# Kernel tuning notes

Measured on AMD Instinct MI355X. Metric: run time of the kernel, lower is better.

## Reference

```python
import jax, jax.numpy as jnp
import numpy as np

B, S, D = 2, 2048, 1024
H = 16
DH = D // H  # 64

def setup_inputs() -> dict:
    key = jax.random.key(0)
    k1, k2, k3, k4 = jax.random.split(key, 4)
    scale = 0.02
    x = jax.random.normal(k1, (B, S, D), dtype=jnp.float32)
    W_query = jax.random.normal(k2, (D, D), dtype=jnp.float32) * scale
    W_key = jax.random.normal(k3, (D, D), dtype=jnp.float32) * scale
    W_value = jax.random.normal(k4, (D, D), dtype=jnp.float32) * scale
    return {"x": x, "W_query": W_query, "W_key": W_key, "W_value": W_value}

def reference(x, W_query, W_key, W_value):
    b, n, d_in = x.shape
    # project and split heads: [b, h, n, dh]
    q = (x @ W_query).reshape(b, n, H, DH).transpose(0, 2, 1, 3)
    k = (x @ W_key).reshape(b, n, H, DH).transpose(0, 2, 1, 3)
    v = (x @ W_value).reshape(b, n, H, DH).transpose(0, 2, 1, 3)
    # raw scores, then causal mask (strict upper triangle -> -inf)
    scores = jnp.einsum('bhqd,bhkd->bhqk', q, k)
    causal = jnp.tril(jnp.ones((n, n), dtype=bool))  # True = keep
    scores = jnp.where(causal, scores, -jnp.inf)
    weights = jax.nn.softmax(scores / jnp.sqrt(jnp.float32(DH)), axis=-1)
    ctx = jnp.einsum('bhqk,bhkd->bhqd', weights, v)
    return ctx.transpose(0, 2, 1, 3).reshape(b, n, H * DH)
```

## Files before the change

kernel.cpp:

```cpp
#include <hip/hip_runtime.h>
#include <hip/hip_bf16.h>

#define S_LEN   2048
#define D_MODEL 1024
#define N_HEADS 16
#define D_HEAD  64
#define HEAD_ELEMS (2048ull * 64ull)
#define MAT_ELEMS  (4096ull * 1024ull)
#define W_ELEMS    (1024ull * 1024ull)

typedef __attribute__((ext_vector_type(8))) short short8_t;
typedef __attribute__((ext_vector_type(4))) short short4_t;
typedef __attribute__((ext_vector_type(4))) float f32x4;

__device__ __forceinline__ short f2bf(float f) {
    __hip_bfloat16 h = __float2bfloat16(f);
    union { __hip_bfloat16 h; short s; } cv;
    cv.h = h;
    return cv.s;
}

#define GLD_LDS16(gptr, lptr) \
    __builtin_amdgcn_global_load_lds( \
        (const __attribute__((address_space(1))) unsigned int*)(gptr), \
        (__attribute__((address_space(3))) unsigned int*)(lptr), 16, 0, 0)

__global__ __launch_bounds__(256) void convert_x_kernel(
    const float* __restrict__ x, short* __restrict__ xb)
{
    const int i = (blockIdx.x * 256 + threadIdx.x) * 8;
    const float4 v0 = *(const float4*)(x + i);
    const float4 v1 = *(const float4*)(x + i + 4);
    short8_t u;
    u[0] = f2bf(v0.x); u[1] = f2bf(v0.y); u[2] = f2bf(v0.z); u[3] = f2bf(v0.w);
    u[4] = f2bf(v1.x); u[5] = f2bf(v1.y); u[6] = f2bf(v1.z); u[7] = f2bf(v1.w);
    *(short8_t*)(xb + i) = u;
}

__global__ __launch_bounds__(256) void transpose_w_kernel(
    const float* __restrict__ Wq, const float* __restrict__ Wk,
    const float* __restrict__ Wv, short* __restrict__ wt)
{
    const int k0 = blockIdx.x * 64;
    const int n0 = blockIdx.y * 64;
    const int which = blockIdx.z;
    const float* W = (which == 0) ? Wq : (which == 1) ? Wk : Wv;
    short* out = wt + (size_t)which * W_ELEMS;

    __shared__ float Ts[64][68];
    const int t = threadIdx.x;
    {
        const int c4 = (t & 15) * 4;
#pragma unroll
        for (int i = 0; i < 4; ++i) {
            const int r = (t >> 4) + i * 16;
            const float4 v = *(const float4*)(W + (size_t)(k0 + r) * D_MODEL + n0 + c4);
            Ts[c4 + 0][r] = v.x; Ts[c4 + 1][r] = v.y;
            Ts[c4 + 2][r] = v.z; Ts[c4 + 3][r] = v.w;
        }
    }
    __syncthreads();
    const int nl = t >> 2;
#pragma unroll
    for (int s = 0; s < 2; ++s) {
        const int koff = (t & 3) * 8 + s * 32;
        short8_t u;
#pragma unroll
        for (int j = 0; j < 8; ++j) u[j] = f2bf(Ts[nl][koff + j]);
        *(short8_t*)(out + (size_t)(n0 + nl) * D_MODEL + k0 + koff) = u;
    }
}

__global__ __launch_bounds__(256, 3) void qkv_mfma_gemm_kernel(
    const short* __restrict__ xb,
    const short* __restrict__ wt,
    short* __restrict__ qkv)
{
    const int mBlock = blockIdx.x * 128;
    const int nBlock = blockIdx.y * 128;
    const int which  = blockIdx.z;
    const short* Bt = wt + (size_t)which * W_ELEMS;
    short* outBase  = qkv + (size_t)which * MAT_ELEMS;

    __shared__ short As[128 * 32];
    __shared__ short Bs[128 * 32];

    const int t    = threadIdx.x;
    const int w    = t >> 6;
    const int lane = t & 63;
    const int n16  = lane & 15;
    const int quad = lane >> 4;
    const int mq   = (w & 1) * 64;
    const int nq   = (w >> 1) * 64;

    f32x4 acc[4][4];
#pragma unroll
    for (int i = 0; i < 4; ++i)
#pragma unroll
        for (int j = 0; j < 4; ++j) acc[i][j] = (f32x4){0.f, 0.f, 0.f, 0.f};

    const int off0 = w * 2048 + lane * 16;
    const int off1 = off0 + 1024;
    const int r0s = off0 >> 6, k0s = (off0 & 63) >> 1;
    const int r1s = off1 >> 6, k1s = (off1 & 63) >> 1;
    const short* gA0 = xb + (size_t)(mBlock + r0s) * D_MODEL + k0s;
    const short* gA1 = xb + (size_t)(mBlock + r1s) * D_MODEL + k1s;
    const short* gB0 = Bt + (size_t)(nBlock + r0s) * D_MODEL + k0s;
    const short* gB1 = Bt + (size_t)(nBlock + r1s) * D_MODEL + k1s;
    short* lA0 = As + w * 1024;
    short* lA1 = As + w * 1024 + 512;
    short* lB0 = Bs + w * 1024;
    short* lB1 = Bs + w * 1024 + 512;

    for (int k0 = 0; k0 < D_MODEL; k0 += 32) {
        __syncthreads();
        GLD_LDS16(gA0 + k0, lA0);
        GLD_LDS16(gA1 + k0, lA1);
        GLD_LDS16(gB0 + k0, lB0);
        GLD_LDS16(gB1 + k0, lB1);
        __syncthreads();

        short8_t af[4], bf[4];
#pragma unroll
        for (int mt = 0; mt < 4; ++mt)
            af[mt] = *(const short8_t*)&As[(mq + mt * 16 + n16) * 32 + quad * 8];
#pragma unroll
        for (int nt = 0; nt < 4; ++nt)
            bf[nt] = *(const short8_t*)&Bs[(nq + nt * 16 + n16) * 32 + quad * 8];
#pragma unroll
        for (int mt = 0; mt < 4; ++mt)
#pragma unroll
            for (int nt = 0; nt < 4; ++nt)
                acc[mt][nt] = __builtin_amdgcn_mfma_f32_16x16x32_bf16(
                    af[mt], bf[nt], acc[mt][nt], 0, 0, 0);
    }

    const float oscale = (which == 0) ? 0.125f : 1.0f;
    if (which < 2) {
#pragma unroll
        for (int mt = 0; mt < 4; ++mt) {
#pragma unroll
            for (int nt = 0; nt < 4; ++nt) {
                const int n = nBlock + nq + nt * 16 + n16;
                const int h = n >> 6, dh = n & 63;
#pragma unroll
                for (int reg = 0; reg < 4; ++reg) {
                    const int m = mBlock + mq + mt * 16 + quad * 4 + reg;
                    const int bb = m >> 11, ss = m & 2047;
                    outBase[((size_t)(bb * N_HEADS + h) * S_LEN + ss) * D_HEAD + dh] =
                        f2bf(acc[mt][nt][reg] * oscale);
                }
            }
        }
    } else {
#pragma unroll
        for (int mt = 0; mt < 4; ++mt) {
            const int m0 = mBlock + mq + mt * 16 + quad * 4;
            const int bb = m0 >> 11, ss0 = m0 & 2047;
#pragma unroll
            for (int nt = 0; nt < 4; ++nt) {
                const int n = nBlock + nq + nt * 16 + n16;
                const int h = n >> 6, dh = n & 63;
                short4_t u;
                u[0] = f2bf(acc[mt][nt][0]); u[1] = f2bf(acc[mt][nt][1]);
                u[2] = f2bf(acc[mt][nt][2]); u[3] = f2bf(acc[mt][nt][3]);
                *(short4_t*)(outBase +
                    ((size_t)((bb * N_HEADS + h) * D_HEAD + dh)) * S_LEN + ss0) = u;
            }
        }
    }
}

__global__ __launch_bounds__(256, 2) void attn_mfma_kernel(
    const short* __restrict__ qkv,
    float* __restrict__ out)
{
    const int bh   = blockIdx.x;
    const int pr   = blockIdx.y;
    const int t    = threadIdx.x;
    const int w    = t >> 6;
    const int lane = t & 63;
    const int n    = lane & 15;
    const int quad = lane >> 4;

    const short* Q  = qkv + (size_t)bh * HEAD_ELEMS;
    const short* K  = qkv + MAT_ELEMS + (size_t)bh * HEAD_ELEMS;
    const short* Vt = qkv + 2 * MAT_ELEMS + (size_t)bh * HEAD_ELEMS;

    __shared__ __align__(16) short Ks[64 * 64];
    __shared__ __align__(16) short Vs[64 * 64];
    __shared__ __align__(16) short Ps[4][16][72];

    const int srow0 = w * 16 + (lane >> 3);
    const int srow1 = srow0 + 8;
    const int sd0 = ((lane & 7) ^ (srow0 & 7)) * 8;
    const int sd1 = ((lane & 7) ^ (srow1 & 7)) * 8;
    const short* gK0 = K + srow0 * 64 + sd0;
    const short* gK1 = K + srow1 * 64 + sd1;
    const short* gV0 = Vt + (size_t)srow0 * S_LEN + sd0;
    const short* gV1 = Vt + (size_t)srow1 * S_LEN + sd1;
    short* lK0 = Ks + (w * 16) * 64;
    short* lK1 = Ks + (w * 16 + 8) * 64;
    short* lV0 = Vs + (w * 16) * 64;
    short* lV1 = Vs + (w * 16 + 8) * 64;

    const int pcK = ((quad ^ (n & 7))) * 8;

    const int bb = bh >> 4;
    const int hh = bh & 15;

    for (int pass = 0; pass < 2; ++pass) {
        const int qb = pass ? (31 - pr) : pr;
        const int r0 = qb * 64 + w * 16;
        const int qrow = r0 + n;

        const short8_t bq0 = *(const short8_t*)(Q + (size_t)qrow * D_HEAD + quad * 8);
        const short8_t bq1 = *(const short8_t*)(Q + (size_t)qrow * D_HEAD + quad * 8 + 32);

        float m = -__builtin_inff();
        float l = 0.f;
        f32x4 o[4];
#pragma unroll
        for (int f = 0; f < 4; ++f) o[f] = (f32x4){0.f, 0.f, 0.f, 0.f};

        for (int tile = 0; tile <= qb; ++tile) {
            const int j0 = tile * 64;
            __syncthreads();
            GLD_LDS16(gK0 + j0 * 64, lK0);
            GLD_LDS16(gK1 + j0 * 64, lK1);
            GLD_LDS16(gV0 + j0, lV0);
            GLD_LDS16(gV1 + j0, lV1);
            __syncthreads();

            f32x4 st[4];
#pragma unroll
            for (int kg = 0; kg < 4; ++kg) {
                const int rbase = (kg * 16 + n) * 64;
                const short8_t a0 = *(const short8_t*)&Ks[rbase + pcK];
                const short8_t a1 = *(const short8_t*)&Ks[rbase + (pcK ^ 32)];
                f32x4 acc = (f32x4){0.f, 0.f, 0.f, 0.f};
                acc = __builtin_amdgcn_mfma_f32_16x16x32_bf16(a0, bq0, acc, 0, 0, 0);
                acc = __builtin_amdgcn_mfma_f32_16x16x32_bf16(a1, bq1, acc, 0, 0, 0);
                st[kg] = acc;
            }

            float p[16];
            float mx = -__builtin_inff();
            if (tile == qb) {
#pragma unroll
                for (int kg = 0; kg < 4; ++kg)
#pragma unroll
                    for (int r = 0; r < 4; ++r) {
                        const int key = j0 + kg * 16 + quad * 4 + r;
                        float s = st[kg][r];
                        s = (key <= qrow) ? s : -__builtin_inff();
                        p[kg * 4 + r] = s;
                        mx = fmaxf(mx, s);
                    }
            } else {
#pragma unroll
                for (int i = 0; i < 16; ++i) {
                    const float s = st[i >> 2][i & 3];
                    p[i] = s;
                    mx = fmaxf(mx, s);
                }
            }
            mx = fmaxf(mx, __shfl_xor(mx, 16));
            mx = fmaxf(mx, __shfl_xor(mx, 32));
            const float mnew  = fmaxf(m, mx);
            const float alpha = __expf(m - mnew);
            float ls = 0.f;
#pragma unroll
            for (int i = 0; i < 16; ++i) {
                p[i] = __expf(p[i] - mnew);
                ls += p[i];
            }
            ls += __shfl_xor(ls, 16);
            ls += __shfl_xor(ls, 32);
            l = l * alpha + ls;
            m = mnew;
#pragma unroll
            for (int f = 0; f < 4; ++f) {
                o[f][0] *= alpha; o[f][1] *= alpha; o[f][2] *= alpha; o[f][3] *= alpha;
            }

#pragma unroll
            for (int kg = 0; kg < 4; ++kg) {
                const unsigned int b0 = __builtin_bit_cast(unsigned int, p[kg * 4 + 0]);
                const unsigned int b1 = __builtin_bit_cast(unsigned int, p[kg * 4 + 1]);
                const unsigned int b2 = __builtin_bit_cast(unsigned int, p[kg * 4 + 2]);
                const unsigned int b3 = __builtin_bit_cast(unsigned int, p[kg * 4 + 3]);
                uint2 pk;
                pk.x = (b0 >> 16) | (b1 & 0xffff0000u);
                pk.y = (b2 >> 16) | (b3 & 0xffff0000u);
                *(uint2*)&Ps[w][n][kg * 16 + quad * 4] = pk;
            }
            const short8_t pb0 = *(const short8_t*)&Ps[w][n][quad * 8];
            const short8_t pb1 = *(const short8_t*)&Ps[w][n][quad * 8 + 32];

#pragma unroll
            for (int f = 0; f < 4; ++f) {
                const int rbase = (f * 16 + n) * 64;
                const short8_t va0 = *(const short8_t*)&Vs[rbase + pcK];
                const short8_t va1 = *(const short8_t*)&Vs[rbase + (pcK ^ 32)];
                o[f] = __builtin_amdgcn_mfma_f32_16x16x32_bf16(va0, pb0, o[f], 0, 0, 0);
                o[f] = __builtin_amdgcn_mfma_f32_16x16x32_bf16(va1, pb1, o[f], 0, 0, 0);
            }
        }

        __syncthreads();
        float* Os = (float*)((w < 2) ? Ks : Vs) + (w & 1) * 1024;
        const float inv_l = 1.0f / l;
#pragma unroll
        for (int f = 0; f < 4; ++f) {
            const int c  = f * 4 + quad;
            const int pc = c ^ n;
            f32x4 q4;
            q4[0] = o[f][0] * inv_l; q4[1] = o[f][1] * inv_l;
            q4[2] = o[f][2] * inv_l; q4[3] = o[f][3] * inv_l;
            *(f32x4*)&Os[n * 64 + pc * 4] = q4;
        }
#pragma unroll
        for (int rr = 0; rr < 4; ++rr) {
            const int row = rr * 4 + quad;
            const int pc  = n ^ row;
            const f32x4 val = *(const f32x4*)&Os[row * 64 + pc * 4];
            *(f32x4*)(out + ((size_t)(bb * S_LEN + r0 + row)) * D_MODEL
                          + hh * D_HEAD + n * 4) = val;
        }
    }
}

extern "C" void kernel_launch(void* const* d_in, const int* in_sizes, int n_in,
                              void* d_out, int out_size, void* d_ws, size_t ws_size,
                              hipStream_t stream) {
    const float* x  = (const float*)d_in[0];
    const float* Wq = (const float*)d_in[1];
    const float* Wk = (const float*)d_in[2];
    const float* Wv = (const float*)d_in[3];
    float* out = (float*)d_out;

    short* xb  = (short*)d_ws;
    short* wt  = xb + MAT_ELEMS;
    short* qkv = wt + 3 * W_ELEMS;

    convert_x_kernel<<<dim3(MAT_ELEMS / (256 * 8)), 256, 0, stream>>>(x, xb);
    transpose_w_kernel<<<dim3(16, 16, 3), 256, 0, stream>>>(Wq, Wk, Wv, wt);

    qkv_mfma_gemm_kernel<<<dim3(32, 8, 3), 256, 0, stream>>>(xb, wt, qkv);

    attn_mfma_kernel<<<dim3(2 * N_HEADS, 16), 256, 0, stream>>>(qkv, out);
}
```

Before: 153.7 us.

## Swap MFMA operands for Q/K vectorized stores; one query block per attention CTA

For the Q and K projections, the GEMM swaps the MFMA A/B operands so each lane holds four consecutive head-dim values and can write them as one 8-byte store, replacing four scalar bf16 stores. The attention kernel drops its two-pass pairing of query blocks (pr and 31-pr) and launches one CTA per query block, 32 per head, raising launch_bounds occupancy to 4. This gives more, shorter CTAs and more concurrency, but workloads become unbalanced under the causal mask, so tail effects depend on scheduling.

```diff
diff --git a/kernel.cpp b/kernel.cpp
--- a/kernel.cpp
+++ b/kernel.cpp
@@ -112,6 +112,7 @@
     short* lB0 = Bs + w * 1024;
     short* lB1 = Bs + w * 1024 + 512;
 
+    const bool swapOp = (which < 2);
     for (int k0 = 0; k0 < D_MODEL; k0 += 32) {
         __syncthreads();
         GLD_LDS16(gA0 + k0, lA0);
@@ -127,29 +128,40 @@
 #pragma unroll
         for (int nt = 0; nt < 4; ++nt)
             bf[nt] = *(const short8_t*)&Bs[(nq + nt * 16 + n16) * 32 + quad * 8];
-#pragma unroll
-        for (int mt = 0; mt < 4; ++mt)
-#pragma unroll
-            for (int nt = 0; nt < 4; ++nt)
-                acc[mt][nt] = __builtin_amdgcn_mfma_f32_16x16x32_bf16(
-                    af[mt], bf[nt], acc[mt][nt], 0, 0, 0);
-    }
-
-    const float oscale = (which == 0) ? 0.125f : 1.0f;
+        if (swapOp) {
+#pragma unroll
+            for (int mt = 0; mt < 4; ++mt)
+#pragma unroll
+                for (int nt = 0; nt < 4; ++nt)
+                    acc[mt][nt] = __builtin_amdgcn_mfma_f32_16x16x32_bf16(
+                        bf[nt], af[mt], acc[mt][nt], 0, 0, 0);
+        } else {
+#pragma unroll
+            for (int mt = 0; mt < 4; ++mt)
+#pragma unroll
+                for (int nt = 0; nt < 4; ++nt)
+                    acc[mt][nt] = __builtin_amdgcn_mfma_f32_16x16x32_bf16(
+                        af[mt], bf[nt], acc[mt][nt], 0, 0, 0);
+        }
+    }
+
     if (which < 2) {
-#pragma unroll
-        for (int mt = 0; mt < 4; ++mt) {
-#pragma unroll
-            for (int nt = 0; nt < 4; ++nt) {
-                const int n = nBlock + nq + nt * 16 + n16;
-                const int h = n >> 6, dh = n & 63;
-#pragma unroll
-                for (int reg = 0; reg < 4; ++reg) {
-                    const int m = mBlock + mq + mt * 16 + quad * 4 + reg;
-                    const int bb = m >> 11, ss = m & 2047;
-                    outBase[((size_t)(bb * N_HEADS + h) * S_LEN + ss) * D_HEAD + dh] =
-                        f2bf(acc[mt][nt][reg] * oscale);
-                }
+        const float oscale = (which == 0) ? 0.125f : 1.0f;
+#pragma unroll
+        for (int nt = 0; nt < 4; ++nt) {
+            const int nBase = nBlock + nq + nt * 16 + quad * 4;
+            const int h = nBase >> 6, dh0 = nBase & 63;
+#pragma unroll
+            for (int mt = 0; mt < 4; ++mt) {
+                const int mrow = mBlock + mq + mt * 16 + n16;
+                const int bb = mrow >> 11, ss = mrow & 2047;
+                short4_t u;
+                u[0] = f2bf(acc[mt][nt][0] * oscale);
+                u[1] = f2bf(acc[mt][nt][1] * oscale);
+                u[2] = f2bf(acc[mt][nt][2] * oscale);
+                u[3] = f2bf(acc[mt][nt][3] * oscale);
+                *(short4_t*)(outBase +
+                    ((size_t)(bb * N_HEADS + h) * S_LEN + ss) * D_HEAD + dh0) = u;
             }
         }
     } else {
@@ -171,12 +183,12 @@
     }
 }
 
-__global__ __launch_bounds__(256, 2) void attn_mfma_kernel(
+__global__ __launch_bounds__(256, 4) void attn_mfma_kernel(
     const short* __restrict__ qkv,
     float* __restrict__ out)
 {
     const int bh   = blockIdx.x;
-    const int pr   = blockIdx.y;
+    const int qb   = blockIdx.y;
     const int t    = threadIdx.x;
     const int w    = t >> 6;
     const int lane = t & 63;
@@ -204,130 +216,127 @@
     short* lV0 = Vs + (w * 16) * 64;
     short* lV1 = Vs + (w * 16 + 8) * 64;
 
-    const int pcK = ((quad ^ (n & 7))) * 8;
+    const int pcK = (quad ^ (n & 7)) * 8;
 
     const int bb = bh >> 4;
     const int hh = bh & 15;
 
-    for (int pass = 0; pass < 2; ++pass) {
-        const int qb = pass ? (31 - pr) : pr;
-        const int r0 = qb * 64 + w * 16;
-        const int qrow = r0 + n;
-
-        const short8_t bq0 = *(const short8_t*)(Q + (size_t)qrow * D_HEAD + quad * 8);
-        const short8_t bq1 = *(const short8_t*)(Q + (size_t)qrow * D_HEAD + quad * 8 + 32);
-
-        float m = -__builtin_inff();
-        float l = 0.f;
-        f32x4 o[4];
-#pragma unroll
-        for (int f = 0; f < 4; ++f) o[f] = (f32x4){0.f, 0.f, 0.f, 0.f};
-
-        for (int tile = 0; tile <= qb; ++tile) {
-            const int j0 = tile * 64;
-            __syncthreads();
-            GLD_LDS16(gK0 + j0 * 64, lK0);
-            GLD_LDS16(gK1 + j0 * 64, lK1);
-            GLD_LDS16(gV0 + j0, lV0);
-            GLD_LDS16(gV1 + j0, lV1);
-            __syncthreads();
-
-            f32x4 st[4];
-#pragma unroll
-            for (int kg = 0; kg < 4; ++kg) {
-                const int rbase = (kg * 16 + n) * 64;
-                const short8_t a0 = *(const short8_t*)&Ks[rbase + pcK];
-                const short8_t a1 = *(const short8_t*)&Ks[rbase + (pcK ^ 32)];
-                f32x4 acc = (f32x4){0.f, 0.f, 0.f, 0.f};
-                acc = __builtin_amdgcn_mfma_f32_16x16x32_bf16(a0, bq0, acc, 0, 0, 0);
-                acc = __builtin_amdgcn_mfma_f32_16x16x32_bf16(a1, bq1, acc, 0, 0, 0);
-                st[kg] = acc;
-            }
-
-            float p[16];
-            float mx = -__builtin_inff();
-            if (tile == qb) {
-#pragma unroll
-                for (int kg = 0; kg < 4; ++kg)
-#pragma unroll
-                    for (int r = 0; r < 4; ++r) {
-                        const int key = j0 + kg * 16 + quad * 4 + r;
-                        float s = st[kg][r];
-                        s = (key <= qrow) ? s : -__builtin_inff();
-                        p[kg * 4 + r] = s;
-                        mx = fmaxf(mx, s);
-                    }
-            } else {
-#pragma unroll
-                for (int i = 0; i < 16; ++i) {
-                    const float s = st[i >> 2][i & 3];
-                    p[i] = s;
+    const int r0 = qb * 64 + w * 16;
+    const int qrow = r0 + n;
+
+    const short8_t bq0 = *(const short8_t*)(Q + (size_t)qrow * D_HEAD + quad * 8);
+    const short8_t bq1 = *(const short8_t*)(Q + (size_t)qrow * D_HEAD + quad * 8 + 32);
+
+    float m = -__builtin_inff();
+    float l = 0.f;
+    f32x4 o[4];
+#pragma unroll
+    for (int f = 0; f < 4; ++f) o[f] = (f32x4){0.f, 0.f, 0.f, 0.f};
+
+    for (int tile = 0; tile <= qb; ++tile) {
+        const int j0 = tile * 64;
+        __syncthreads();
+        GLD_LDS16(gK0 + j0 * 64, lK0);
+        GLD_LDS16(gK1 + j0 * 64, lK1);
+        GLD_LDS16(gV0 + j0, lV0);
+        GLD_LDS16(gV1 + j0, lV1);
+        __syncthreads();
+
+        f32x4 st[4];
+#pragma unroll
+        for (int kg = 0; kg < 4; ++kg) {
+            const int rbase = (kg * 16 + n) * 64;
+            const short8_t a0 = *(const short8_t*)&Ks[rbase + pcK];
+            const short8_t a1 = *(const short8_t*)&Ks[rbase + (pcK ^ 32)];
+            f32x4 acc = (f32x4){0.f, 0.f, 0.f, 0.f};
+            acc = __builtin_amdgcn_mfma_f32_16x16x32_bf16(a0, bq0, acc, 0, 0, 0);
+            acc = __builtin_amdgcn_mfma_f32_16x16x32_bf16(a1, bq1, acc, 0, 0, 0);
+            st[kg] = acc;
+        }
+
+        float p[16];
+        float mx = -__builtin_inff();
+        if (tile == qb) {
+#pragma unroll
+            for (int kg = 0; kg < 4; ++kg)
+#pragma unroll
+                for (int r = 0; r < 4; ++r) {
+                    const int key = j0 + kg * 16 + quad * 4 + r;
+                    float s = st[kg][r];
+                    s = (key <= qrow) ? s : -__builtin_inff();
+                    p[kg * 4 + r] = s;
                     mx = fmaxf(mx, s);
                 }
+        } else {
+#pragma unroll
+            for (int i = 0; i < 16; ++i) {
+                const float s = st[i >> 2][i & 3];
+                p[i] = s;
+                mx = fmaxf(mx, s);
             }
-            mx = fmaxf(mx, __shfl_xor(mx, 16));
-            mx = fmaxf(mx, __shfl_xor(mx, 32));
-            const float mnew  = fmaxf(m, mx);
-            const float alpha = __expf(m - mnew);
-            float ls = 0.f;
-#pragma unroll
-            for (int i = 0; i < 16; ++i) {
-                p[i] = __expf(p[i] - mnew);
-                ls += p[i];
-            }
-            ls += __shfl_xor(ls, 16);
-            ls += __shfl_xor(ls, 32);
-            l = l * alpha + ls;
-            m = mnew;
-#pragma unroll
-            for (int f = 0; f < 4; ++f) {
-                o[f][0] *= alpha; o[f][1] *= alpha; o[f][2] *= alpha; o[f][3] *= alpha;
-            }
-
-#pragma unroll
-            for (int kg = 0; kg < 4; ++kg) {
-                const unsigned int b0 = __builtin_bit_cast(unsigned int, p[kg * 4 + 0]);
-                const unsigned int b1 = __builtin_bit_cast(unsigned int, p[kg * 4 + 1]);
-                const unsigned int b2 = __builtin_bit_cast(unsigned int, p[kg * 4 + 2]);
-                const unsigned int b3 = __builtin_bit_cast(unsigned int, p[kg * 4 + 3]);
-                uint2 pk;
-                pk.x = (b0 >> 16) | (b1 & 0xffff0000u);
-                pk.y = (b2 >> 16) | (b3 & 0xffff0000u);
-                *(uint2*)&Ps[w][n][kg * 16 + quad * 4] = pk;
-            }
-            const short8_t pb0 = *(const short8_t*)&Ps[w][n][quad * 8];
-            const short8_t pb1 = *(const short8_t*)&Ps[w][n][quad * 8 + 32];
-
-#pragma unroll
-            for (int f = 0; f < 4; ++f) {
-                const int rbase = (f * 16 + n) * 64;
-                const short8_t va0 = *(const short8_t*)&Vs[rbase + pcK];
-                const short8_t va1 = *(const short8_t*)&Vs[rbase + (pcK ^ 32)];
-                o[f] = __builtin_amdgcn_mfma_f32_16x16x32_bf16(va0, pb0, o[f], 0, 0, 0);
-                o[f] = __builtin_amdgcn_mfma_f32_16x16x32_bf16(va1, pb1, o[f], 0, 0, 0);
-            }
-        }
-
-        __syncthreads();
-        float* Os = (float*)((w < 2) ? Ks : Vs) + (w & 1) * 1024;
-        const float inv_l = 1.0f / l;
+        }
+        mx = fmaxf(mx, __shfl_xor(mx, 16));
+        mx = fmaxf(mx, __shfl_xor(mx, 32));
+        const float mnew  = fmaxf(m, mx);
+        const float alpha = __expf(m - mnew);
+        float ls = 0.f;
+#pragma unroll
+        for (int i = 0; i < 16; ++i) {
+            p[i] = __expf(p[i] - mnew);
+            ls += p[i];
+        }
+        ls += __shfl_xor(ls, 16);
+        ls += __shfl_xor(ls, 32);
+        l = l * alpha + ls;
+        m = mnew;
 #pragma unroll
         for (int f = 0; f < 4; ++f) {
-            const int c  = f * 4 + quad;
-            const int pc = c ^ n;
-            f32x4 q4;
-            q4[0] = o[f][0] * inv_l; q4[1] = o[f][1] * inv_l;
-            q4[2] = o[f][2] * inv_l; q4[3] = o[f][3] * inv_l;
-            *(f32x4*)&Os[n * 64 + pc * 4] = q4;
-        }
-#pragma unroll
-        for (int rr = 0; rr < 4; ++rr) {
-            const int row = rr * 4 + quad;
-            const int pc  = n ^ row;
-            const f32x4 val = *(const f32x4*)&Os[row * 64 + pc * 4];
-            *(f32x4*)(out + ((size_t)(bb * S_LEN + r0 + row)) * D_MODEL
-                          + hh * D_HEAD + n * 4) = val;
-        }
+            o[f][0] *= alpha; o[f][1] *= alpha; o[f][2] *= alpha; o[f][3] *= alpha;
+        }
+
+#pragma unroll
+        for (int kg = 0; kg < 4; ++kg) {
+            const unsigned int b0 = __builtin_bit_cast(unsigned int, p[kg * 4 + 0]);
+            const unsigned int b1 = __builtin_bit_cast(unsigned int, p[kg * 4 + 1]);
+            const unsigned int b2 = __builtin_bit_cast(unsigned int, p[kg * 4 + 2]);
+            const unsigned int b3 = __builtin_bit_cast(unsigned int, p[kg * 4 + 3]);
+            uint2 pk;
+            pk.x = (b0 >> 16) | (b1 & 0xffff0000u);
+            pk.y = (b2 >> 16) | (b3 & 0xffff0000u);
+            *(uint2*)&Ps[w][n][kg * 16 + quad * 4] = pk;
+        }
+        const short8_t pb0 = *(const short8_t*)&Ps[w][n][quad * 8];
+        const short8_t pb1 = *(const short8_t*)&Ps[w][n][quad * 8 + 32];
+
+#pragma unroll
+        for (int f = 0; f < 4; ++f) {
+            const int rbase = (f * 16 + n) * 64;
+            const short8_t va0 = *(const short8_t*)&Vs[rbase + pcK];
+            const short8_t va1 = *(const short8_t*)&Vs[rbase + (pcK ^ 32)];
+            o[f] = __builtin_amdgcn_mfma_f32_16x16x32_bf16(va0, pb0, o[f], 0, 0, 0);
+            o[f] = __builtin_amdgcn_mfma_f32_16x16x32_bf16(va1, pb1, o[f], 0, 0, 0);
+        }
+    }
+
+    __syncthreads();
+    float* Os = (float*)((w < 2) ? Ks : Vs) + (w & 1) * 1024;
+    const float inv_l = 1.0f / l;
+#pragma unroll
+    for (int f = 0; f < 4; ++f) {
+        const int c  = f * 4 + quad;
+        const int pc = c ^ n;
+        f32x4 q4;
+        q4[0] = o[f][0] * inv_l; q4[1] = o[f][1] * inv_l;
+        q4[2] = o[f][2] * inv_l; q4[3] = o[f][3] * inv_l;
+        *(f32x4*)&Os[n * 64 + pc * 4] = q4;
+    }
+#pragma unroll
+    for (int rr = 0; rr < 4; ++rr) {
+        const int row = rr * 4 + quad;
+        const int pc  = n ^ row;
+        const f32x4 val = *(const f32x4*)&Os[row * 64 + pc * 4];
+        *(f32x4*)(out + ((size_t)(bb * S_LEN + r0 + row)) * D_MODEL
+                      + hh * D_HEAD + n * 4) = val;
     }
 }
 
@@ -349,5 +358,5 @@
 
     qkv_mfma_gemm_kernel<<<dim3(32, 8, 3), 256, 0, stream>>>(xb, wt, qkv);
 
-    attn_mfma_kernel<<<dim3(2 * N_HEADS, 16), 256, 0, stream>>>(qkv, out);
-}
+    attn_mfma_kernel<<<dim3(2 * N_HEADS, S_LEN / 64), 256, 0, stream>>>(qkv, out);
+}
```

After: 209.0 us. 1.36x slower.

## Double-buffer K/V tiles in attention and fold log2e into Q scale

Applied to the files above, without the earlier changes.

The attention loop now holds two K/V buffers in LDS. It issues the async global-to-LDS loads for tile t+1 before computing on tile t, with one barrier per tile instead of two. The goal is to hide global memory latency behind the MFMA and softmax work. The Q projection scale now includes log2(e), so the softmax can call exp2f directly and skip one multiply per exponential. The cost is double the K/V LDS footprint, which may limit occupancy.

```diff
diff --git a/kernel.cpp b/kernel.cpp
--- a/kernel.cpp
+++ b/kernel.cpp
@@ -135,7 +135,7 @@
                     af[mt], bf[nt], acc[mt][nt], 0, 0, 0);
     }
 
-    const float oscale = (which == 0) ? 0.125f : 1.0f;
+    const float oscale = (which == 0) ? 0.18033688f : 1.0f;
     if (which < 2) {
 #pragma unroll
         for (int mt = 0; mt < 4; ++mt) {
@@ -187,8 +187,8 @@
     const short* K  = qkv + MAT_ELEMS + (size_t)bh * HEAD_ELEMS;
     const short* Vt = qkv + 2 * MAT_ELEMS + (size_t)bh * HEAD_ELEMS;
 
-    __shared__ __align__(16) short Ks[64 * 64];
-    __shared__ __align__(16) short Vs[64 * 64];
+    __shared__ __align__(16) short Ks[2 * 64 * 64];
+    __shared__ __align__(16) short Vs[2 * 64 * 64];
     __shared__ __align__(16) short Ps[4][16][72];
 
     const int srow0 = w * 16 + (lane >> 3);
@@ -204,7 +204,7 @@
     short* lV0 = Vs + (w * 16) * 64;
     short* lV1 = Vs + (w * 16 + 8) * 64;
 
-    const int pcK = ((quad ^ (n & 7))) * 8;
+    const int pcK = (quad ^ (n & 7)) * 8;
 
     const int bb = bh >> 4;
     const int hh = bh & 15;
@@ -223,19 +223,31 @@
 #pragma unroll
         for (int f = 0; f < 4; ++f) o[f] = (f32x4){0.f, 0.f, 0.f, 0.f};
 
+        __syncthreads();
+        GLD_LDS16(gK0, lK0);
+        GLD_LDS16(gK1, lK1);
+        GLD_LDS16(gV0, lV0);
+        GLD_LDS16(gV1, lV1);
+
         for (int tile = 0; tile <= qb; ++tile) {
+            const int cur = (tile & 1) * 4096;
+            __syncthreads();
+
+            if (tile < qb) {
+                const int nxt = ((tile + 1) & 1) * 4096;
+                const int j1 = (tile + 1) * 64;
+                GLD_LDS16(gK0 + j1 * 64, lK0 + nxt);
+                GLD_LDS16(gK1 + j1 * 64, lK1 + nxt);
+                GLD_LDS16(gV0 + j1, lV0 + nxt);
+                GLD_LDS16(gV1 + j1, lV1 + nxt);
+            }
+
             const int j0 = tile * 64;
-            __syncthreads();
-            GLD_LDS16(gK0 + j0 * 64, lK0);
-            GLD_LDS16(gK1 + j0 * 64, lK1);
-            GLD_LDS16(gV0 + j0, lV0);
-            GLD_LDS16(gV1 + j0, lV1);
-            __syncthreads();
 
             f32x4 st[4];
 #pragma unroll
             for (int kg = 0; kg < 4; ++kg) {
-                const int rbase = (kg * 16 + n) * 64;
+                const int rbase = cur + (kg * 16 + n) * 64;
                 const short8_t a0 = *(const short8_t*)&Ks[rbase + pcK];
                 const short8_t a1 = *(const short8_t*)&Ks[rbase + (pcK ^ 32)];
                 f32x4 acc = (f32x4){0.f, 0.f, 0.f, 0.f};
@@ -268,11 +280,11 @@
             mx = fmaxf(mx, __shfl_xor(mx, 16));
             mx = fmaxf(mx, __shfl_xor(mx, 32));
             const float mnew  = fmaxf(m, mx);
-            const float alpha = __expf(m - mnew);
+            const float alpha = exp2f(m - mnew);
             float ls = 0.f;
 #pragma unroll
             for (int i = 0; i < 16; ++i) {
-                p[i] = __expf(p[i] - mnew);
+                p[i] = exp2f(p[i] - mnew);
                 ls += p[i];
             }
             ls += __shfl_xor(ls, 16);
@@ -300,7 +312,7 @@
 
 #pragma unroll
             for (int f = 0; f < 4; ++f) {
-                const int rbase = (f * 16 + n) * 64;
+                const int rbase = cur + (f * 16 + n) * 64;
                 const short8_t va0 = *(const short8_t*)&Vs[rbase + pcK];
                 const short8_t va1 = *(const short8_t*)&Vs[rbase + (pcK ^ 32)];
                 o[f] = __builtin_amdgcn_mfma_f32_16x16x32_bf16(va0, pb0, o[f], 0, 0, 0);
```

New measurement: 160.4 us. 1.04x slower.
